# Kernel optimization log

Hardware: AMD Instinct MI355X
Metric: run time of the kernel (lower is better)

## Reference

```python
import jax, jax.numpy as jnp
import numpy as np

K = 9      # kernel size
DIL = 2    # dilation
PAD = 8    # padding -> same-size output


def unfold(x):
    """nd2col: (B,C,H,W) -> (B,C,K,K,H,W) patches with dilation/padding."""
    B, C, H, W = x.shape
    xp = jnp.pad(x, ((0, 0), (0, 0), (PAD, PAD), (PAD, PAD)))
    cols = jnp.stack(
        [xp[:, :, i * DIL:i * DIL + H, j * DIL:j * DIL + W]
         for i in range(K) for j in range(K)], axis=2)
    return cols.reshape(B, C, K, K, H, W)


def pac_kernel(f):
    """Gaussian adaptive kernel: exp(-0.5*||f_nbr - f_center||^2), shape (B,1,K,K,H,W)."""
    # center of the dilated patch (K//2, K//2) is the pixel itself
    d = unfold(f) - f[:, :, None, None, :, :]
    return jnp.exp(-0.5 * jnp.sum(d * d, axis=1, keepdims=True))


def pacconv(x, k, w, b):
    """Pixel-adaptive conv: unfold, modulate by guidance kernel, contract with weight."""
    cols = unfold(x)                                  # (B,Cin,K,K,H,W)
    out = jnp.einsum('bcklhw,ockl->bohw', cols * k, w)
    return out + b[None, :, None, None]


def setup_inputs() -> dict:
    key = jax.random.key(0)
    ks = jax.random.split(key, 6)
    B, C, H, W = 1, 32, 128, 128
    x = jax.random.normal(ks[0], (B, C, H, W), jnp.float32)
    f = jax.random.normal(ks[1], (B, C, H, W), jnp.float32)
    fan_in = C * K * K
    bound = float(1.0 / np.sqrt(fan_in))
    W1 = jax.random.uniform(ks[2], (32, C, K, K), jnp.float32, -bound, bound)
    b1 = jax.random.uniform(ks[3], (32,), jnp.float32, -bound, bound)
    W2 = jax.random.uniform(ks[4], (32, 32, K, K), jnp.float32, -bound, bound)
    b2 = jax.random.uniform(ks[5], (32,), jnp.float32, -bound, bound)
    return {"x": x, "f": f, "W1": W1, "b1": b1, "W2": W2, "b2": b2}


def reference(x, f, W1, b1, W2, b2):
    k = pac_kernel(f)  # same guidance for both layers -> identical kernel
    h = pacconv(x, k, W1, b1)
    return pacconv(h, k, W2, b2)
```

## Files before the change

kernel.cpp:

```cpp
#include <hip/hip_runtime.h>

#define HH 128
#define WW 128
#define NPIX 16384
#define NC 32
#define NO 32
#define KS 9
#define TAPS 81
#define DIL 2
#define PAD 8
#define SMAX 27.6310211159f
#define NW (NO * NC * TAPS)
#define OG 16
#define OPG 2

__global__ __launch_bounds__(256) void prep_k_kernel(
    const float* __restrict__ f,
    const float* __restrict__ W1, const float* __restrict__ W2,
    float* __restrict__ kbuf, unsigned short* __restrict__ mask9,
    float* __restrict__ W1t, float* __restrict__ W2t)
{
    const int i = blockIdx.y;
    if (i == KS) {
        for (int t = blockIdx.x * 256 + threadIdx.x; t < NW; t += 64 * 256) {
            int o = t / (NC * TAPS);
            int r = t - o * (NC * TAPS);
            int c = r / TAPS;
            int tap = r - c * TAPS;
            int d = (tap * NO + o) * NC + c;
            W1t[d] = W1[t];
            W2t[d] = W2[t];
        }
        return;
    }
    const int pix = blockIdx.x * 256 + threadIdx.x;
    const int h = pix >> 7, w = pix & (WW - 1);

    float fc[NC];
#pragma unroll
    for (int c = 0; c < NC; ++c) fc[c] = f[c * NPIX + pix];

    const int qh = h + i * DIL - PAD;
    const bool vh = (unsigned)qh < HH;
    unsigned pmask = 0;
#pragma unroll
    for (int j = 0; j < KS; ++j) {
        int qw = w + j * DIL - PAD;
        bool valid = vh & ((unsigned)qw < WW);
        int q = valid ? (qh * WW + qw) : pix;
        float s0 = 0.f, s1 = 0.f, s2 = 0.f, s3 = 0.f;
#pragma unroll
        for (int c4 = 0; c4 < 8; ++c4) {
            float d0 = f[(4 * c4 + 0) * NPIX + q] - fc[4 * c4 + 0];
            float d1 = f[(4 * c4 + 1) * NPIX + q] - fc[4 * c4 + 1];
            float d2 = f[(4 * c4 + 2) * NPIX + q] - fc[4 * c4 + 2];
            float d3 = f[(4 * c4 + 3) * NPIX + q] - fc[4 * c4 + 3];
            s0 = fmaf(d0, d0, s0); s1 = fmaf(d1, d1, s1);
            s2 = fmaf(d2, d2, s2); s3 = fmaf(d3, d3, s3);
        }
        float s = (s0 + s1) + (s2 + s3);
        bool live = valid && (s <= SMAX) && !(i == 4 && j == 4);
        if (live) {
            pmask |= 1u << j;
            kbuf[(i * KS + j) * NPIX + pix] = __expf(-0.5f * s);
        }
    }
    mask9[i * NPIX + pix] = (unsigned short)pmask;
}

__global__ __launch_bounds__(256) void pac_kernel(
    const float* __restrict__ in, const float* __restrict__ kbuf,
    const unsigned short* __restrict__ mask9, const float* __restrict__ Wt,
    const float* __restrict__ bias, float* __restrict__ out)
{
    const int pix = blockIdx.x * 256 + threadIdx.x;
    const int ob = blockIdx.y * OPG;

    unsigned long long M0 = 0ull;
    unsigned M1;
#pragma unroll
    for (int i = 0; i < 7; ++i)
        M0 |= (unsigned long long)mask9[i * NPIX + pix] << (9 * i);
    {
        unsigned mk7 = mask9[7 * NPIX + pix];
        unsigned mk8 = mask9[8 * NPIX + pix];
        M0 |= (unsigned long long)(mk7 & 1u) << 63;
        M1 = (mk7 >> 1) | (mk8 << 8);
    }

    const float* __restrict__ wc = Wt + (40 * NO + ob) * NC;
    float a0 = 0.f, a1 = 0.f;
    {
        float x0[NC];
#pragma unroll
        for (int c = 0; c < NC; ++c) x0[c] = in[c * NPIX + pix];
#pragma unroll
        for (int c = 0; c < NC; ++c) {
            a0 = fmaf(x0[c], wc[c], a0);
            a1 = fmaf(x0[c], wc[NC + c], a1);
        }
    }

#define SPARSE_TAP(T) do {                                                 \
        int ii_ = (T) / 9, jj_ = (T) - 9 * ii_;                            \
        int q_ = pix + (ii_ * DIL - PAD) * WW + (jj_ * DIL - PAD);         \
        float kv_ = kbuf[(T) * NPIX + pix];                                \
        const float* wp_ = Wt + ((T) * NO + ob) * NC;                      \
        float t0_ = 0.f, t1_ = 0.f;                                        \
        _Pragma("unroll")                                                  \
        for (int c = 0; c < NC; ++c) {                                     \
            float xv_ = in[c * NPIX + q_];                                 \
            t0_ = fmaf(xv_, wp_[c], t0_);                                  \
            t1_ = fmaf(xv_, wp_[NC + c], t1_);                             \
        }                                                                  \
        a0 = fmaf(kv_, t0_, a0);                                           \
        a1 = fmaf(kv_, t1_, a1);                                           \
    } while (0)

    while (M0) {
        int t = __builtin_ctzll(M0);
        M0 &= M0 - 1;
        SPARSE_TAP(t);
    }
    while (M1) {
        int t = 64 + __builtin_ctz(M1);
        M1 &= M1 - 1;
        SPARSE_TAP(t);
    }
#undef SPARSE_TAP

    out[(ob + 0) * NPIX + pix] = a0 + bias[ob + 0];
    out[(ob + 1) * NPIX + pix] = a1 + bias[ob + 1];
}

#define CHUNK 27
#define NCHUNK 3
#define KMIN 1e-6f
__global__ __launch_bounds__(256) void pac_layer_fuse(
    const float* __restrict__ in, const float* __restrict__ f,
    const float* __restrict__ Wt, const float* __restrict__ bias,
    float* __restrict__ out)
{
    __shared__ float wl[NC * CHUNK * 8];
    const int og = blockIdx.y;
    const int pix = blockIdx.x * 256 + threadIdx.x;
    const int h = pix >> 7, w = pix & (WW - 1);
    float acc[8];
#pragma unroll
    for (int i = 0; i < 8; ++i) acc[i] = 0.f;
    float fc[NC];
#pragma unroll
    for (int c = 0; c < NC; ++c) fc[c] = f[c * NPIX + pix];
    for (int ch = 0; ch < NCHUNK; ++ch) {
        __syncthreads();
        for (int idx = threadIdx.x; idx < NC * CHUNK * 8; idx += 256) {
            int t = idx % CHUNK;
            int c = (idx / CHUNK) % NC;
            int o = idx / (CHUNK * NC);
            wl[(c * CHUNK + t) * 8 + o] =
                Wt[(og * 8 + o) * (NC * TAPS) + c * TAPS + ch * CHUNK + t];
        }
        __syncthreads();
        for (int t = 0; t < CHUNK; ++t) {
            int tap = ch * CHUNK + t;
            int qh = h + (tap / KS) * DIL - PAD;
            int qw = w + (tap % KS) * DIL - PAD;
            bool valid = ((unsigned)qh < HH) & ((unsigned)qw < WW);
            int q = qh * WW + qw;
            float s = 0.f;
#pragma unroll
            for (int c = 0; c < NC; ++c) {
                float fn = valid ? f[c * NPIX + q] : 0.f;
                float d = fn - fc[c];
                s = fmaf(d, d, s);
            }
            float kv = __expf(-0.5f * s);
            if (__all((kv < KMIN) | (!valid))) continue;
            const float* wpp = &wl[t * 8];
#pragma unroll 8
            for (int c = 0; c < NC; ++c) {
                float v = valid ? in[c * NPIX + q] : 0.f;
                v *= kv;
#pragma unroll
                for (int o = 0; o < 8; ++o)
                    acc[o] = fmaf(v, wpp[c * CHUNK * 8 + o], acc[o]);
            }
        }
    }
#pragma unroll
    for (int o = 0; o < 8; ++o)
        out[(og * 8 + o) * NPIX + pix] = acc[o] + bias[og * 8 + o];
}

extern "C" void kernel_launch(void* const* d_in, const int* in_sizes, int n_in,
                              void* d_out, int out_size, void* d_ws, size_t ws_size,
                              hipStream_t stream)
{
    (void)in_sizes; (void)n_in; (void)out_size;
    const float* x  = (const float*)d_in[0];
    const float* f  = (const float*)d_in[1];
    const float* W1 = (const float*)d_in[2];
    const float* b1 = (const float*)d_in[3];
    const float* W2 = (const float*)d_in[4];
    const float* b2 = (const float*)d_in[5];
    float* out = (float*)d_out;

    float* ws = (float*)d_ws;
    float* kbuf = ws;
    unsigned short* mask9 = (unsigned short*)(ws + TAPS * NPIX);
    float* W1t = ws + TAPS * NPIX + (KS * NPIX) / 2;
    float* W2t = W1t + NW;
    float* ht  = W2t + NW;
    const size_t need =
        (size_t)(TAPS * NPIX + (KS * NPIX) / 2 + 2 * NW + NO * NPIX) * sizeof(float);

    if (ws_size >= need) {
        prep_k_kernel<<<dim3(64, KS + 1), 256, 0, stream>>>(
            f, W1, W2, kbuf, mask9, W1t, W2t);
        pac_kernel<<<dim3(64, OG), 256, 0, stream>>>(x,  kbuf, mask9, W1t, b1, ht);
        pac_kernel<<<dim3(64, OG), 256, 0, stream>>>(ht, kbuf, mask9, W2t, b2, out);
    } else {
        float* hbuf = ws;
        pac_layer_fuse<<<dim3(64, 4), 256, 0, stream>>>(x, f, W1, b1, hbuf);
        pac_layer_fuse<<<dim3(64, 4), 256, 0, stream>>>(hbuf, f, W2, b2, out);
    }
}
```

Baseline: 119.9 us.

## Replace per-pixel tap bitmask with compacted global sparse tap list and atomics

```diff
diff --git a/kernel.cpp b/kernel.cpp
--- a/kernel.cpp
+++ b/kernel.cpp
@@ -10,29 +10,41 @@
 #define DIL 2
 #define PAD 8
 #define SMAX 27.6310211159f
-#define NW (NO * NC * TAPS)
-#define OG 16
-#define OPG 2
-
-__global__ __launch_bounds__(256) void prep_k_kernel(
-    const float* __restrict__ f,
-    const float* __restrict__ W1, const float* __restrict__ W2,
-    float* __restrict__ kbuf, unsigned short* __restrict__ mask9,
-    float* __restrict__ W1t, float* __restrict__ W2t)
+#define CAP 262144
+
+__global__ __launch_bounds__(256) void dense_center(
+    const float* __restrict__ in, const float* __restrict__ W,
+    const float* __restrict__ bias, float* __restrict__ out,
+    unsigned* __restrict__ cnt)
+{
+    if (cnt && blockIdx.x == 0 && blockIdx.y == 0 && threadIdx.x == 0) *cnt = 0u;
+    const int pix = blockIdx.x * 256 + threadIdx.x;
+    const int o0 = blockIdx.y * 4;
+
+    float x0[NC];
+#pragma unroll
+    for (int c = 0; c < NC; ++c) x0[c] = in[c * NPIX + pix];
+
+    float a0 = 0.f, a1 = 0.f, a2 = 0.f, a3 = 0.f;
+#pragma unroll
+    for (int c = 0; c < NC; ++c) {
+        float xv = x0[c];
+        a0 = fmaf(xv, W[((o0 + 0) * NC + c) * TAPS + 40], a0);
+        a1 = fmaf(xv, W[((o0 + 1) * NC + c) * TAPS + 40], a1);
+        a2 = fmaf(xv, W[((o0 + 2) * NC + c) * TAPS + 40], a2);
+        a3 = fmaf(xv, W[((o0 + 3) * NC + c) * TAPS + 40], a3);
+    }
+    out[(o0 + 0) * NPIX + pix] = a0 + bias[o0 + 0];
+    out[(o0 + 1) * NPIX + pix] = a1 + bias[o0 + 1];
+    out[(o0 + 2) * NPIX + pix] = a2 + bias[o0 + 2];
+    out[(o0 + 3) * NPIX + pix] = a3 + bias[o0 + 3];
+}
+
+__global__ __launch_bounds__(256) void prep_list(
+    const float* __restrict__ f, unsigned* __restrict__ cnt,
+    unsigned* __restrict__ meta, float* __restrict__ kvl)
 {
     const int i = blockIdx.y;
-    if (i == KS) {
-        for (int t = blockIdx.x * 256 + threadIdx.x; t < NW; t += 64 * 256) {
-            int o = t / (NC * TAPS);
-            int r = t - o * (NC * TAPS);
-            int c = r / TAPS;
-            int tap = r - c * TAPS;
-            int d = (tap * NO + o) * NC + c;
-            W1t[d] = W1[t];
-            W2t[d] = W2[t];
-        }
-        return;
-    }
     const int pix = blockIdx.x * 256 + threadIdx.x;
     const int h = pix >> 7, w = pix & (WW - 1);
 
@@ -42,7 +54,6 @@
 
     const int qh = h + i * DIL - PAD;
     const bool vh = (unsigned)qh < HH;
-    unsigned pmask = 0;
 #pragma unroll
     for (int j = 0; j < KS; ++j) {
         int qw = w + j * DIL - PAD;
@@ -61,76 +72,44 @@
         float s = (s0 + s1) + (s2 + s3);
         bool live = valid && (s <= SMAX) && !(i == 4 && j == 4);
         if (live) {
-            pmask |= 1u << j;
-            kbuf[(i * KS + j) * NPIX + pix] = __expf(-0.5f * s);
-        }
-    }
-    mask9[i * NPIX + pix] = (unsigned short)pmask;
-}
-
-__global__ __launch_bounds__(256) void pac_kernel(
-    const float* __restrict__ in, const float* __restrict__ kbuf,
-    const unsigned short* __restrict__ mask9, const float* __restrict__ Wt,
-    const float* __restrict__ bias, float* __restrict__ out)
-{
-    const int pix = blockIdx.x * 256 + threadIdx.x;
-    const int ob = blockIdx.y * OPG;
-
-    unsigned long long M0 = 0ull;
-    unsigned M1;
-#pragma unroll
-    for (int i = 0; i < 7; ++i)
-        M0 |= (unsigned long long)mask9[i * NPIX + pix] << (9 * i);
-    {
-        unsigned mk7 = mask9[7 * NPIX + pix];
-        unsigned mk8 = mask9[8 * NPIX + pix];
-        M0 |= (unsigned long long)(mk7 & 1u) << 63;
-        M1 = (mk7 >> 1) | (mk8 << 8);
-    }
-
-    const float* __restrict__ wc = Wt + (40 * NO + ob) * NC;
-    float a0 = 0.f, a1 = 0.f;
-    {
-        float x0[NC];
-#pragma unroll
-        for (int c = 0; c < NC; ++c) x0[c] = in[c * NPIX + pix];
-#pragma unroll
-        for (int c = 0; c < NC; ++c) {
-            a0 = fmaf(x0[c], wc[c], a0);
-            a1 = fmaf(x0[c], wc[NC + c], a1);
-        }
-    }
-
-#define SPARSE_TAP(T) do {                                                 \
-        int ii_ = (T) / 9, jj_ = (T) - 9 * ii_;                            \
-        int q_ = pix + (ii_ * DIL - PAD) * WW + (jj_ * DIL - PAD);         \
-        float kv_ = kbuf[(T) * NPIX + pix];                                \
-        const float* wp_ = Wt + ((T) * NO + ob) * NC;                      \
-        float t0_ = 0.f, t1_ = 0.f;                                        \
-        _Pragma("unroll")                                                  \
-        for (int c = 0; c < NC; ++c) {                                     \
-            float xv_ = in[c * NPIX + q_];                                 \
-            t0_ = fmaf(xv_, wp_[c], t0_);                                  \
-            t1_ = fmaf(xv_, wp_[NC + c], t1_);                             \
-        }                                                                  \
-        a0 = fmaf(kv_, t0_, a0);                                           \
-        a1 = fmaf(kv_, t1_, a1);                                           \
-    } while (0)
-
-    while (M0) {
-        int t = __builtin_ctzll(M0);
-        M0 &= M0 - 1;
-        SPARSE_TAP(t);
-    }
-    while (M1) {
-        int t = 64 + __builtin_ctz(M1);
-        M1 &= M1 - 1;
-        SPARSE_TAP(t);
-    }
-#undef SPARSE_TAP
-
-    out[(ob + 0) * NPIX + pix] = a0 + bias[ob + 0];
-    out[(ob + 1) * NPIX + pix] = a1 + bias[ob + 1];
+            unsigned idx = atomicAdd(cnt, 1u);
+            if (idx < CAP) {
+                meta[idx] = (unsigned)pix | ((unsigned)(i * KS + j) << 14);
+                kvl[idx] = __expf(-0.5f * s);
+            }
+        }
+    }
+}
+
+__global__ __launch_bounds__(256) void sparse_resid(
+    const float* __restrict__ in, const float* __restrict__ W,
+    const unsigned* __restrict__ cnt, const unsigned* __restrict__ meta,
+    const float* __restrict__ kvl, float* __restrict__ out)
+{
+    unsigned n = *cnt;
+    if (n > CAP) n = CAP;
+    const unsigned total = n * 32u;
+    for (unsigned it = blockIdx.x * 256 + threadIdx.x; it < total;
+         it += gridDim.x * 256) {
+        unsigned e = it >> 5;
+        int o = (int)(it & 31u);
+        unsigned m = meta[e];
+        int pix = (int)(m & 16383u);
+        int T = (int)(m >> 14);
+        int ii = T / KS, jj = T - KS * ii;
+        int q = pix + (ii * DIL - PAD) * WW + (jj * DIL - PAD);
+        float kv = kvl[e];
+        const float* __restrict__ wp = W + o * (NC * TAPS) + T;
+        float t0 = 0.f, t1 = 0.f, t2 = 0.f, t3 = 0.f;
+#pragma unroll
+        for (int c4 = 0; c4 < 8; ++c4) {
+            t0 = fmaf(in[(4 * c4 + 0) * NPIX + q], wp[(4 * c4 + 0) * TAPS], t0);
+            t1 = fmaf(in[(4 * c4 + 1) * NPIX + q], wp[(4 * c4 + 1) * TAPS], t1);
+            t2 = fmaf(in[(4 * c4 + 2) * NPIX + q], wp[(4 * c4 + 2) * TAPS], t2);
+            t3 = fmaf(in[(4 * c4 + 3) * NPIX + q], wp[(4 * c4 + 3) * TAPS], t3);
+        }
+        atomicAdd(&out[o * NPIX + pix], kv * ((t0 + t1) + (t2 + t3)));
+    }
 }
 
 #define CHUNK 27
@@ -206,19 +185,18 @@
     float* out = (float*)d_out;
 
     float* ws = (float*)d_ws;
-    float* kbuf = ws;
-    unsigned short* mask9 = (unsigned short*)(ws + TAPS * NPIX);
-    float* W1t = ws + TAPS * NPIX + (KS * NPIX) / 2;
-    float* W2t = W1t + NW;
-    float* ht  = W2t + NW;
-    const size_t need =
-        (size_t)(TAPS * NPIX + (KS * NPIX) / 2 + 2 * NW + NO * NPIX) * sizeof(float);
+    float* hbufm = ws;
+    unsigned* cnt  = (unsigned*)(ws + NO * NPIX);
+    unsigned* meta = cnt + 4;
+    float* kvl = (float*)(meta + CAP);
+    const size_t need = (size_t)(NO * NPIX + 4 + 2 * CAP) * 4;
 
     if (ws_size >= need) {
-        prep_k_kernel<<<dim3(64, KS + 1), 256, 0, stream>>>(
-            f, W1, W2, kbuf, mask9, W1t, W2t);
-        pac_kernel<<<dim3(64, OG), 256, 0, stream>>>(x,  kbuf, mask9, W1t, b1, ht);
-        pac_kernel<<<dim3(64, OG), 256, 0, stream>>>(ht, kbuf, mask9, W2t, b2, out);
+        dense_center<<<dim3(64, 8), 256, 0, stream>>>(x, W1, b1, hbufm, cnt);
+        prep_list<<<dim3(64, KS), 256, 0, stream>>>(f, cnt, meta, kvl);
+        sparse_resid<<<dim3(384), 256, 0, stream>>>(x, W1, cnt, meta, kvl, hbufm);
+        dense_center<<<dim3(64, 8), 256, 0, stream>>>(hbufm, W2, b2, out, nullptr);
+        sparse_resid<<<dim3(384), 256, 0, stream>>>(hbufm, W2, cnt, meta, kvl, out);
     } else {
         float* hbuf = ws;
         pac_layer_fuse<<<dim3(64, 4), 256, 0, stream>>>(x, f, W1, b1, hbuf);
```

After: 144.4 us. 20.3% more time.
